# Kernel tuning notes

Hardware: AMD Instinct MI355X
Metric: run time of the kernel (lower is better)

The kernel has to match this reference:

```python
import jax, jax.numpy as jnp
import numpy as np

N_LEVELS = 16
N_FEATS = 2
LOG2_T = 19
TABLE_SIZE = 2 ** LOG2_T
BASE_RES = 16
PER_LEVEL_SCALE = 1.3819
N_PTS = 524288
# per-level grid resolutions (static)
RESOLUTIONS = np.floor(BASE_RES * PER_LEVEL_SCALE ** np.arange(N_LEVELS)).astype(np.float32)
# NGP spatial hash primes for 2D
PRIME0 = np.uint32(1)
PRIME1 = np.uint32(2654435761)
# corner offsets for bilinear interp: (0,0),(0,1),(1,0),(1,1)
CORNER_OFFS = np.array([[0, 0], [0, 1], [1, 0], [1, 1]], dtype=np.uint32)


def setup_inputs() -> dict:
    key = jax.random.key(0)
    k1, k2 = jax.random.split(key)
    pts = jax.random.uniform(k1, (N_PTS, 3), dtype=jnp.float32)  # coords in [0,1]
    # 3 planes x L levels x T entries x F features, small init like NGP (1e-4)
    tables = jax.random.normal(k2, (3, N_LEVELS, TABLE_SIZE, N_FEATS), dtype=jnp.float32) * 1e-4
    return {"pts": pts, "tables": tables}


def _encode_plane(coords, table):
    # coords: [N,2] in [0,1]; table: [L,T,F]
    L, T, F = table.shape
    res = jnp.asarray(RESOLUTIONS)  # [L]
    scaled = coords[None, :, :] * res[:, None, None]  # [L,N,2]
    x0 = jnp.floor(scaled)
    frac = scaled - x0  # [L,N,2]
    x0u = x0.astype(jnp.uint32)
    offs = jnp.asarray(CORNER_OFFS)  # [4,2]
    corners = x0u[:, :, None, :] + offs[None, None, :, :]  # [L,N,4,2]
    # NGP spatial hash with uint32 wraparound, then mod table size
    h = (corners[..., 0] * PRIME0) ^ (corners[..., 1] * PRIME1)  # [L,N,4] uint32
    idx = (h % jnp.uint32(T)).astype(jnp.int32)  # [L,N,4]
    feats = table[jnp.arange(L)[:, None, None], idx]  # [L,N,4,F]
    # bilinear weights: product over dims of frac (offset=1) or 1-frac (offset=0)
    fo = offs.astype(coords.dtype)  # [4,2]
    w = jnp.prod(jnp.where(fo[None, None] > 0, frac[:, :, None, :], 1.0 - frac[:, :, None, :]), axis=-1)  # [L,N,4]
    out = jnp.einsum('lnc,lncf->lnf', w, feats)  # [L,N,F]
    return out.transpose(1, 0, 2).reshape(coords.shape[0], L * F)  # [N, L*F]


def reference(pts, tables):
    # coordinate-pair planes: combinations of (0,1,2) taken 2 at a time
    coo_combs = [(0, 1), (0, 2), (1, 2)]
    interp_space = 1.0
    for ci, comb in enumerate(coo_combs):
        interp_space = interp_space * _encode_plane(pts[:, list(comb)], tables[ci])
    return interp_space  # [N, 32]
```

## Files before the change

### kernel.cpp

```cpp
#include <hip/hip_runtime.h>
#include <stdint.h>


#define NPTS   524288u
#define TSIZE  524288u
#define TMASK  0x7FFFFu
#define PRIME1 2654435761u

__constant__ float c_res[16] = {
    16.f, 22.f, 30.f, 42.f, 58.f, 80.f, 111.f, 153.f,
    212.f, 294.f, 406.f, 561.f, 775.f, 1072.f, 1481.f, 2047.f
};
__constant__ int c_resi[6] = {16, 22, 30, 42, 58, 80};

__constant__ uint16_t c_mid_lo[6]  = {0, 56, 0, 39, 78, 117};
__constant__ uint16_t c_mid_hiX[6] = {56, 112, 39, 78, 117, 154};

__global__ __launch_bounds__(512) void kplane_lds(
    const float* __restrict__ pts,
    const float2* __restrict__ tab,
    float2* __restrict__ ws)
{
    __shared__ float2 sm[6561];
    const uint32_t b     = blockIdx.x;
    const uint32_t gidx  = b >> 6;
    const uint32_t chunk = b & 63u;
    const uint32_t plane = gidx / 6u;
    const uint32_t lvl   = gidx - plane * 6u;
    const uint32_t g     = plane * 16u + lvl;
    const uint32_t R     = (uint32_t)c_resi[lvl] + 1u;
    const uint32_t E     = R * R;
    const float    res   = c_res[lvl];
    const uint32_t base  = g * TSIZE;
    const uint32_t t     = threadIdx.x;

    for (uint32_t i = t; i < E; i += 512u) {
        const uint32_t cx = i / R;
        const uint32_t cy = i - cx * R;
        sm[i] = tab[base + ((cx ^ (cy * PRIME1)) & TMASK)];
    }
    __syncthreads();

    const uint32_t c0  = (plane == 2u) ? 1u : 0u;
    const uint32_t c1  = (plane == 0u) ? 1u : 2u;
    const uint32_t pt0 = chunk * 8192u + t;

#pragma unroll 4
    for (uint32_t k = 0; k < 16u; ++k) {
        const uint32_t pt = pt0 + k * 512u;
        const float s0 = pts[pt * 3u + c0] * res;
        const float s1 = pts[pt * 3u + c1] * res;
        const float f0 = floorf(s0);
        const float f1 = floorf(s1);
        const float r0 = s0 - f0;
        const float r1 = s1 - f1;
        const uint32_t ci = (uint32_t)f0 * R + (uint32_t)f1;
        const float2 q00 = sm[ci];
        const float2 q01 = sm[ci + 1u];
        const float2 q10 = sm[ci + R];
        const float2 q11 = sm[ci + R + 1u];
        const float w00 = (1.f - r0) * (1.f - r1);
        const float w01 = (1.f - r0) * r1;
        const float w10 = r0 * (1.f - r1);
        const float w11 = r0 * r1;
        ws[g * NPTS + pt] = make_float2(
            w00 * q00.x + w01 * q01.x + w10 * q10.x + w11 * q11.x,
            w00 * q00.y + w01 * q01.y + w10 * q10.y + w11 * q11.y);
    }
}

__global__ __launch_bounds__(512) void kplane_mid(
    const float* __restrict__ pts,
    const float2* __restrict__ tab,
    float2* __restrict__ ws)
{
    __shared__ float2 sm[6400];
    const uint32_t b     = blockIdx.x;
    const uint32_t sg    = b >> 5;
    const uint32_t chunk = b & 31u;
    const uint32_t plane = sg / 6u;
    const uint32_t local = sg - plane * 6u;
    const uint32_t lvl   = (local < 2u) ? 6u : 7u;
    const uint32_t g     = plane * 16u + lvl;
    const uint32_t R     = (lvl == 6u) ? 112u : 154u;
    const uint32_t lo    = c_mid_lo[local];
    const uint32_t hiX   = c_mid_hiX[local];
    const uint32_t nrows = ((hiX < R ? hiX : R - 1u) - lo) + 1u;
    const uint32_t E     = nrows * R;
    const float    res   = c_res[lvl];
    const uint32_t base  = g * TSIZE;
    const uint32_t t     = threadIdx.x;

    for (uint32_t i = t; i < E; i += 512u) {
        const uint32_t rr = i / R;
        const uint32_t cy = i - rr * R;
        const uint32_t cx = lo + rr;
        sm[i] = tab[base + ((cx ^ (cy * PRIME1)) & TMASK)];
    }
    __syncthreads();

    const uint32_t c0  = (plane == 2u) ? 1u : 0u;
    const uint32_t c1  = (plane == 0u) ? 1u : 2u;
    const uint32_t pt0 = chunk * 16384u + t;

#pragma unroll 4
    for (uint32_t k = 0; k < 32u; ++k) {
        const uint32_t pt = pt0 + k * 512u;
        const float s0 = pts[pt * 3u + c0] * res;
        const float s1 = pts[pt * 3u + c1] * res;
        const float f0 = floorf(s0);
        const float f1 = floorf(s1);
        const uint32_t u0 = (uint32_t)f0;
        if (u0 >= lo && u0 < hiX) {
            const float r0 = s0 - f0;
            const float r1 = s1 - f1;
            const uint32_t ci = (u0 - lo) * R + (uint32_t)f1;
            const float2 q00 = sm[ci];
            const float2 q01 = sm[ci + 1u];
            const float2 q10 = sm[ci + R];
            const float2 q11 = sm[ci + R + 1u];
            const float w00 = (1.f - r0) * (1.f - r1);
            const float w01 = (1.f - r0) * r1;
            const float w10 = r0 * (1.f - r1);
            const float w11 = r0 * r1;
            ws[g * NPTS + pt] = make_float2(
                w00 * q00.x + w01 * q01.x + w10 * q10.x + w11 * q11.x,
                w00 * q00.y + w01 * q01.y + w10 * q10.y + w11 * q11.y);
        }
    }
}

__global__ __launch_bounds__(256) void kplane_hi(
    const float* __restrict__ pts,
    const float2* __restrict__ tab,
    float2* __restrict__ ws)
{
    const uint32_t b     = blockIdx.x;
    const uint32_t xcd   = b & 7u;
    const uint32_t s     = b >> 3;
    const uint32_t phase = s >> 9;
    const uint32_t chunk = s & 511u;
    const uint32_t plane = phase;
    const uint32_t lvl   = 8u + ((xcd + 3u * phase) & 7u);
    const uint32_t g     = plane * 16u + lvl;
    const float    res   = c_res[lvl];
    const uint32_t c0    = (plane == 2u) ? 1u : 0u;
    const uint32_t c1    = (plane == 0u) ? 1u : 2u;
    const uint32_t base  = g * TSIZE;
    const float4* __restrict__ tab4 = (const float4*)tab;
    const uint32_t b4    = g * (TSIZE / 2u);
    const uint32_t pt0   = chunk * 1024u + threadIdx.x;

    float4 P0[4], P1[4];
    float2 Q0[4], Q1[4];
    float  r0[4], r1[4];
    uint32_t sel0[4], sel1[4], oddm[4];

#pragma unroll
    for (int k = 0; k < 4; ++k) {
        const uint32_t pt = pt0 + (uint32_t)k * 256u;
        const float s0 = pts[pt * 3u + c0] * res;
        const float s1 = pts[pt * 3u + c1] * res;
        const float f0 = floorf(s0);
        const float f1 = floorf(s1);
        r0[k] = s0 - f0;
        r1[k] = s1 - f1;
        const uint32_t u0  = (uint32_t)f0;
        const uint32_t hy0 = (uint32_t)f1 * PRIME1;
        const uint32_t hy1 = hy0 + PRIME1;
        const uint32_t i00 = ( u0        ^ hy0) & TMASK;
        const uint32_t i01 = ( u0        ^ hy1) & TMASK;
        const uint32_t i10 = ((u0 + 1u)  ^ hy0) & TMASK;
        const uint32_t i11 = ((u0 + 1u)  ^ hy1) & TMASK;
        sel0[k] = i00 & 1u;
        sel1[k] = i01 & 1u;
        oddm[k] = u0 & 1u;
        P0[k] = tab4[b4 + (i00 >> 1)];
        P1[k] = tab4[b4 + (i01 >> 1)];
        Q0[k] = make_float2(0.f, 0.f);
        Q1[k] = make_float2(0.f, 0.f);
        if (oddm[k]) {
            Q0[k] = tab[base + i10];
            Q1[k] = tab[base + i11];
        }
    }
#pragma unroll
    for (int k = 0; k < 4; ++k) {
        const uint32_t pt = pt0 + (uint32_t)k * 256u;
        const float2 lo0 = make_float2(P0[k].x, P0[k].y);
        const float2 hi0 = make_float2(P0[k].z, P0[k].w);
        const float2 lo1 = make_float2(P1[k].x, P1[k].y);
        const float2 hi1 = make_float2(P1[k].z, P1[k].w);
        const float2 t00 = sel0[k] ? hi0 : lo0;
        const float2 t01 = sel1[k] ? hi1 : lo1;
        const float2 t10 = oddm[k] ? Q0[k] : (sel0[k] ? lo0 : hi0);
        const float2 t11 = oddm[k] ? Q1[k] : (sel1[k] ? lo1 : hi1);
        const float w00 = (1.f - r0[k]) * (1.f - r1[k]);
        const float w01 = (1.f - r0[k]) * r1[k];
        const float w10 = r0[k] * (1.f - r1[k]);
        const float w11 = r0[k] * r1[k];
        ws[g * NPTS + pt] = make_float2(
            w00 * t00.x + w01 * t01.x + w10 * t10.x + w11 * t11.x,
            w00 * t00.y + w01 * t01.y + w10 * t10.y + w11 * t11.y);
    }
}

__global__ __launch_bounds__(256) void kplane_combine(
    const float2* __restrict__ ws,
    float2* __restrict__ out)
{
    __shared__ float2 tile[16][65];
    const uint32_t pt0 = blockIdx.x * 64u;
    const uint32_t t   = threadIdx.x;
    const uint32_t lr  = t >> 6;
    const uint32_t ptl = t & 63u;

#pragma unroll
    for (int k = 0; k < 4; ++k) {
        const uint32_t lvl = (uint32_t)k * 4u + lr;
        const float2 a = ws[( 0u + lvl) * NPTS + pt0 + ptl];
        const float2 b = ws[(16u + lvl) * NPTS + pt0 + ptl];
        const float2 c = ws[(32u + lvl) * NPTS + pt0 + ptl];
        tile[lvl][ptl] = make_float2(a.x * b.x * c.x, a.y * b.y * c.y);
    }
    __syncthreads();
#pragma unroll
    for (int k = 0; k < 4; ++k) {
        const uint32_t e      = t + (uint32_t)k * 256u;
        const uint32_t out_lv = e & 15u;
        const uint32_t out_pt = e >> 4;
        out[(pt0 + out_pt) * 16u + out_lv] = tile[out_lv][out_pt];
    }
}

template <int P, bool FIRST>
__global__ __launch_bounds__(256) void kplane_pass(
    const float* __restrict__ pts,
    const float2* __restrict__ tab,
    float2* __restrict__ ws)
{
    const uint32_t b     = blockIdx.x;
    const uint32_t xcd   = b & 7u;
    const uint32_t s     = b >> 3;
    const uint32_t gi    = s >> 11;
    const uint32_t chunk = s & 2047u;
    const uint32_t lvl   = gi * 8u + xcd;
    const uint32_t pt    = chunk * 256u + threadIdx.x;

    constexpr int c0 = (P == 2) ? 1 : 0;
    constexpr int c1 = (P == 0) ? 1 : 2;

    const float a0  = pts[pt * 3u + c0];
    const float a1  = pts[pt * 3u + c1];
    const float res = c_res[lvl];

    const float s0 = a0 * res;
    const float s1 = a1 * res;
    const float f0 = floorf(s0);
    const float f1 = floorf(s1);
    const float r0 = s0 - f0;
    const float r1 = s1 - f1;
    const uint32_t u0 = (uint32_t)f0;
    const uint32_t hy0  = (uint32_t)f1 * PRIME1;
    const uint32_t hy1  = hy0 + PRIME1;
    const uint32_t base = ((uint32_t)P * 16u + lvl) * TSIZE;

    const float2 t00 = tab[base + (( u0       ^ hy0) & TMASK)];
    const float2 t01 = tab[base + (( u0       ^ hy1) & TMASK)];
    const float2 t10 = tab[base + (((u0 + 1u) ^ hy0) & TMASK)];
    const float2 t11 = tab[base + (((u0 + 1u) ^ hy1) & TMASK)];

    const float w00 = (1.f - r0) * (1.f - r1);
    const float w01 = (1.f - r0) * r1;
    const float w10 = r0 * (1.f - r1);
    const float w11 = r0 * r1;

    const float e0 = w00 * t00.x + w01 * t01.x + w10 * t10.x + w11 * t11.x;
    const float e1 = w00 * t00.y + w01 * t01.y + w10 * t10.y + w11 * t11.y;

    const uint32_t widx = lvl * NPTS + pt;
    if (FIRST) {
        ws[widx] = make_float2(e0, e1);
    } else {
        const float2 prev = ws[widx];
        ws[widx] = make_float2(prev.x * e0, prev.y * e1);
    }
}

__global__ __launch_bounds__(256) void kplane_transpose(
    const float2* __restrict__ ws, float2* __restrict__ out)
{
    const uint32_t tid = blockIdx.x * 256u + threadIdx.x;
    const uint32_t lvl = tid & 15u;
    const uint32_t pt  = tid >> 4;
    out[tid] = ws[lvl * NPTS + pt];
}

extern "C" void kernel_launch(void* const* d_in, const int* in_sizes, int n_in,
                              void* d_out, int out_size, void* d_ws, size_t ws_size,
                              hipStream_t stream) {
    const float*  pts = (const float*)d_in[0];
    const float2* tab = (const float2*)d_in[1];
    float2*       out = (float2*)d_out;

    const size_t wsA = (size_t)48 * NPTS * sizeof(float2);
    const size_t wsB = (size_t)16 * NPTS * sizeof(float2);
    dim3 block256(256u), block512(512u);

    if (ws_size >= wsA) {
        float2* ws = (float2*)d_ws;
        dim3 hgrid(3u * 8u * 512u);
        hipLaunchKernelGGL(kplane_hi, hgrid, block256, 0, stream, pts, tab, ws);
        dim3 mgrid(18u * 32u);
        hipLaunchKernelGGL(kplane_mid, mgrid, block512, 0, stream, pts, tab, ws);
        dim3 lgrid(18u * 64u);
        hipLaunchKernelGGL(kplane_lds, lgrid, block512, 0, stream, pts, tab, ws);
        dim3 cgrid(NPTS / 64u);
        hipLaunchKernelGGL(kplane_combine, cgrid, block256, 0, stream, ws, out);
    } else if (ws_size >= wsB) {
        float2* ws = (float2*)d_ws;
        dim3 grid(16u * (NPTS / 256u));
        hipLaunchKernelGGL((kplane_pass<0, true >), grid, block256, 0, stream, pts, tab, ws);
        hipLaunchKernelGGL((kplane_pass<1, false>), grid, block256, 0, stream, pts, tab, ws);
        hipLaunchKernelGGL((kplane_pass<2, false>), grid, block256, 0, stream, pts, tab, ws);
        dim3 tgrid((NPTS * 16u) / 256u);
        hipLaunchKernelGGL(kplane_transpose, tgrid, block256, 0, stream, ws, out);
    }
}
```

Before: 277.2 us.

## Pack plane coordinates and merge mid/low-level LDS kernels into one launch

Adds a pre-pass that repacks the xyz points into three per-plane float2 arrays, stored temporarily in the output buffer, so the gather kernels load coordinates with one contiguous 8-byte read. The separate mid-level and low-level LDS kernels are merged into a single launch. Levels 0-4 of each plane share one block that stages all five small grids in LDS and reuses each loaded point across them, while level 5 and levels 6-7 keep their own blocks with more points per block. A fallback monolithic kernel is added for small workspaces. The aim is fewer launches, less redundant point traffic and less LDS fill work, at the cost of an extra pack pass and fewer, longer-running blocks that may underfill the GPU.

```diff
diff --git a/kernel.cpp b/kernel.cpp
--- a/kernel.cpp
+++ b/kernel.cpp
@@ -11,127 +11,28 @@
     16.f, 22.f, 30.f, 42.f, 58.f, 80.f, 111.f, 153.f,
     212.f, 294.f, 406.f, 561.f, 775.f, 1072.f, 1481.f, 2047.f
 };
-__constant__ int c_resi[6] = {16, 22, 30, 42, 58, 80};
+
+__constant__ int c_RA[5]   = {17, 23, 31, 43, 59};
+__constant__ int c_offA[5] = {0, 289, 818, 1779, 3628};
 
 __constant__ uint16_t c_mid_lo[6]  = {0, 56, 0, 39, 78, 117};
 __constant__ uint16_t c_mid_hiX[6] = {56, 112, 39, 78, 117, 154};
 
-__global__ __launch_bounds__(512) void kplane_lds(
+__global__ __launch_bounds__(256) void kplane_pack(
     const float* __restrict__ pts,
-    const float2* __restrict__ tab,
-    float2* __restrict__ ws)
-{
-    __shared__ float2 sm[6561];
-    const uint32_t b     = blockIdx.x;
-    const uint32_t gidx  = b >> 6;
-    const uint32_t chunk = b & 63u;
-    const uint32_t plane = gidx / 6u;
-    const uint32_t lvl   = gidx - plane * 6u;
-    const uint32_t g     = plane * 16u + lvl;
-    const uint32_t R     = (uint32_t)c_resi[lvl] + 1u;
-    const uint32_t E     = R * R;
-    const float    res   = c_res[lvl];
-    const uint32_t base  = g * TSIZE;
-    const uint32_t t     = threadIdx.x;
-
-    for (uint32_t i = t; i < E; i += 512u) {
-        const uint32_t cx = i / R;
-        const uint32_t cy = i - cx * R;
-        sm[i] = tab[base + ((cx ^ (cy * PRIME1)) & TMASK)];
-    }
-    __syncthreads();
-
-    const uint32_t c0  = (plane == 2u) ? 1u : 0u;
-    const uint32_t c1  = (plane == 0u) ? 1u : 2u;
-    const uint32_t pt0 = chunk * 8192u + t;
-
-#pragma unroll 4
-    for (uint32_t k = 0; k < 16u; ++k) {
-        const uint32_t pt = pt0 + k * 512u;
-        const float s0 = pts[pt * 3u + c0] * res;
-        const float s1 = pts[pt * 3u + c1] * res;
-        const float f0 = floorf(s0);
-        const float f1 = floorf(s1);
-        const float r0 = s0 - f0;
-        const float r1 = s1 - f1;
-        const uint32_t ci = (uint32_t)f0 * R + (uint32_t)f1;
-        const float2 q00 = sm[ci];
-        const float2 q01 = sm[ci + 1u];
-        const float2 q10 = sm[ci + R];
-        const float2 q11 = sm[ci + R + 1u];
-        const float w00 = (1.f - r0) * (1.f - r1);
-        const float w01 = (1.f - r0) * r1;
-        const float w10 = r0 * (1.f - r1);
-        const float w11 = r0 * r1;
-        ws[g * NPTS + pt] = make_float2(
-            w00 * q00.x + w01 * q01.x + w10 * q10.x + w11 * q11.x,
-            w00 * q00.y + w01 * q01.y + w10 * q10.y + w11 * q11.y);
-    }
-}
-
-__global__ __launch_bounds__(512) void kplane_mid(
-    const float* __restrict__ pts,
-    const float2* __restrict__ tab,
-    float2* __restrict__ ws)
-{
-    __shared__ float2 sm[6400];
-    const uint32_t b     = blockIdx.x;
-    const uint32_t sg    = b >> 5;
-    const uint32_t chunk = b & 31u;
-    const uint32_t plane = sg / 6u;
-    const uint32_t local = sg - plane * 6u;
-    const uint32_t lvl   = (local < 2u) ? 6u : 7u;
-    const uint32_t g     = plane * 16u + lvl;
-    const uint32_t R     = (lvl == 6u) ? 112u : 154u;
-    const uint32_t lo    = c_mid_lo[local];
-    const uint32_t hiX   = c_mid_hiX[local];
-    const uint32_t nrows = ((hiX < R ? hiX : R - 1u) - lo) + 1u;
-    const uint32_t E     = nrows * R;
-    const float    res   = c_res[lvl];
-    const uint32_t base  = g * TSIZE;
-    const uint32_t t     = threadIdx.x;
-
-    for (uint32_t i = t; i < E; i += 512u) {
-        const uint32_t rr = i / R;
-        const uint32_t cy = i - rr * R;
-        const uint32_t cx = lo + rr;
-        sm[i] = tab[base + ((cx ^ (cy * PRIME1)) & TMASK)];
-    }
-    __syncthreads();
-
-    const uint32_t c0  = (plane == 2u) ? 1u : 0u;
-    const uint32_t c1  = (plane == 0u) ? 1u : 2u;
-    const uint32_t pt0 = chunk * 16384u + t;
-
-#pragma unroll 4
-    for (uint32_t k = 0; k < 32u; ++k) {
-        const uint32_t pt = pt0 + k * 512u;
-        const float s0 = pts[pt * 3u + c0] * res;
-        const float s1 = pts[pt * 3u + c1] * res;
-        const float f0 = floorf(s0);
-        const float f1 = floorf(s1);
-        const uint32_t u0 = (uint32_t)f0;
-        if (u0 >= lo && u0 < hiX) {
-            const float r0 = s0 - f0;
-            const float r1 = s1 - f1;
-            const uint32_t ci = (u0 - lo) * R + (uint32_t)f1;
-            const float2 q00 = sm[ci];
-            const float2 q01 = sm[ci + 1u];
-            const float2 q10 = sm[ci + R];
-            const float2 q11 = sm[ci + R + 1u];
-            const float w00 = (1.f - r0) * (1.f - r1);
-            const float w01 = (1.f - r0) * r1;
-            const float w10 = r0 * (1.f - r1);
-            const float w11 = r0 * r1;
-            ws[g * NPTS + pt] = make_float2(
-                w00 * q00.x + w01 * q01.x + w10 * q10.x + w11 * q11.x,
-                w00 * q00.y + w01 * q01.y + w10 * q10.y + w11 * q11.y);
-        }
-    }
+    float2* __restrict__ pts2)
+{
+    const uint32_t pt = blockIdx.x * 256u + threadIdx.x;
+    const float x = pts[pt * 3u + 0u];
+    const float y = pts[pt * 3u + 1u];
+    const float z = pts[pt * 3u + 2u];
+    pts2[            pt] = make_float2(x, y);
+    pts2[NPTS      + pt] = make_float2(x, z);
+    pts2[2u * NPTS + pt] = make_float2(y, z);
 }
 
 __global__ __launch_bounds__(256) void kplane_hi(
-    const float* __restrict__ pts,
+    const float2* __restrict__ pts2,
     const float2* __restrict__ tab,
     float2* __restrict__ ws)
 {
@@ -144,12 +45,11 @@
     const uint32_t lvl   = 8u + ((xcd + 3u * phase) & 7u);
     const uint32_t g     = plane * 16u + lvl;
     const float    res   = c_res[lvl];
-    const uint32_t c0    = (plane == 2u) ? 1u : 0u;
-    const uint32_t c1    = (plane == 0u) ? 1u : 2u;
     const uint32_t base  = g * TSIZE;
     const float4* __restrict__ tab4 = (const float4*)tab;
     const uint32_t b4    = g * (TSIZE / 2u);
     const uint32_t pt0   = chunk * 1024u + threadIdx.x;
+    const float2* __restrict__ pp = pts2 + (size_t)plane * NPTS;
 
     float4 P0[4], P1[4];
     float2 Q0[4], Q1[4];
@@ -159,8 +59,9 @@
 #pragma unroll
     for (int k = 0; k < 4; ++k) {
         const uint32_t pt = pt0 + (uint32_t)k * 256u;
-        const float s0 = pts[pt * 3u + c0] * res;
-        const float s1 = pts[pt * 3u + c1] * res;
+        const float2 c2 = pp[pt];
+        const float s0 = c2.x * res;
+        const float s1 = c2.y * res;
         const float f0 = floorf(s0);
         const float f1 = floorf(s1);
         r0[k] = s0 - f0;
@@ -205,6 +106,164 @@
     }
 }
 
+__global__ __launch_bounds__(512) void kplane_midlds(
+    const float2* __restrict__ pts2,
+    const float2* __restrict__ tab,
+    float2* __restrict__ ws)
+{
+    __shared__ float2 sm[7109];
+    const uint32_t b = blockIdx.x;
+    const uint32_t t = threadIdx.x;
+
+    if (b < 288u) {
+        const uint32_t sg    = b >> 4;
+        const uint32_t chunk = b & 15u;
+        const uint32_t plane = sg / 6u;
+        const uint32_t local = sg - plane * 6u;
+        const uint32_t lvl   = (local < 2u) ? 6u : 7u;
+        const uint32_t g     = plane * 16u + lvl;
+        const uint32_t R     = (lvl == 6u) ? 112u : 154u;
+        const uint32_t lo    = c_mid_lo[local];
+        const uint32_t hiX   = c_mid_hiX[local];
+        const uint32_t nrows = ((hiX < R ? hiX : R - 1u) - lo) + 1u;
+        const uint32_t E     = nrows * R;
+        const float    res   = c_res[lvl];
+        const uint32_t base  = g * TSIZE;
+
+        for (uint32_t i = t; i < E; i += 512u) {
+            const uint32_t rr = i / R;
+            const uint32_t cy = i - rr * R;
+            const uint32_t cx = lo + rr;
+            sm[i] = tab[base + ((cx ^ (cy * PRIME1)) & TMASK)];
+        }
+        __syncthreads();
+
+        const float2* __restrict__ pp = pts2 + (size_t)plane * NPTS;
+        const uint32_t pt0 = chunk * 32768u + t;
+
+#pragma unroll 4
+        for (uint32_t k = 0; k < 64u; ++k) {
+            const uint32_t pt = pt0 + k * 512u;
+            const float2 c2 = pp[pt];
+            const float s0 = c2.x * res;
+            const float s1 = c2.y * res;
+            const float f0 = floorf(s0);
+            const float f1 = floorf(s1);
+            const uint32_t u0 = (uint32_t)f0;
+            if (u0 >= lo && u0 < hiX) {
+                const float r0 = s0 - f0;
+                const float r1 = s1 - f1;
+                const uint32_t ci = (u0 - lo) * R + (uint32_t)f1;
+                const float2 q00 = sm[ci];
+                const float2 q01 = sm[ci + 1u];
+                const float2 q10 = sm[ci + R];
+                const float2 q11 = sm[ci + R + 1u];
+                const float w00 = (1.f - r0) * (1.f - r1);
+                const float w01 = (1.f - r0) * r1;
+                const float w10 = r0 * (1.f - r1);
+                const float w11 = r0 * r1;
+                ws[g * NPTS + pt] = make_float2(
+                    w00 * q00.x + w01 * q01.x + w10 * q10.x + w11 * q11.x,
+                    w00 * q00.y + w01 * q01.y + w10 * q10.y + w11 * q11.y);
+            }
+        }
+    } else if (b < 336u) {
+        const uint32_t idx   = b - 288u;
+        const uint32_t plane = idx >> 4;
+        const uint32_t chunk = idx & 15u;
+
+#pragma unroll
+        for (int l = 0; l < 5; ++l) {
+            const uint32_t R    = (uint32_t)c_RA[l];
+            const uint32_t E    = R * R;
+            const uint32_t off  = (uint32_t)c_offA[l];
+            const uint32_t base = (plane * 16u + (uint32_t)l) * TSIZE;
+            for (uint32_t i = t; i < E; i += 512u) {
+                const uint32_t cx = i / R;
+                const uint32_t cy = i - cx * R;
+                sm[off + i] = tab[base + ((cx ^ (cy * PRIME1)) & TMASK)];
+            }
+        }
+        __syncthreads();
+
+        const float2* __restrict__ pp = pts2 + (size_t)plane * NPTS;
+        const uint32_t pt0 = chunk * 32768u + t;
+
+#pragma unroll 2
+        for (uint32_t k = 0; k < 64u; ++k) {
+            const uint32_t pt = pt0 + k * 512u;
+            const float2 c2 = pp[pt];
+#pragma unroll
+            for (int l = 0; l < 5; ++l) {
+                const uint32_t R   = (uint32_t)c_RA[l];
+                const uint32_t off = (uint32_t)c_offA[l];
+                const float res = c_res[l];
+                const float s0 = c2.x * res;
+                const float s1 = c2.y * res;
+                const float f0 = floorf(s0);
+                const float f1 = floorf(s1);
+                const float r0 = s0 - f0;
+                const float r1 = s1 - f1;
+                const uint32_t ci = off + (uint32_t)f0 * R + (uint32_t)f1;
+                const float2 q00 = sm[ci];
+                const float2 q01 = sm[ci + 1u];
+                const float2 q10 = sm[ci + R];
+                const float2 q11 = sm[ci + R + 1u];
+                const float w00 = (1.f - r0) * (1.f - r1);
+                const float w01 = (1.f - r0) * r1;
+                const float w10 = r0 * (1.f - r1);
+                const float w11 = r0 * r1;
+                ws[(plane * 16u + (uint32_t)l) * NPTS + pt] = make_float2(
+                    w00 * q00.x + w01 * q01.x + w10 * q10.x + w11 * q11.x,
+                    w00 * q00.y + w01 * q01.y + w10 * q10.y + w11 * q11.y);
+            }
+        }
+    } else {
+        const uint32_t idx   = b - 336u;
+        const uint32_t plane = idx >> 4;
+        const uint32_t chunk = idx & 15u;
+        const uint32_t R     = 81u;
+        const uint32_t E     = 6561u;
+        const float    res   = 80.f;
+        const uint32_t g     = plane * 16u + 5u;
+        const uint32_t base  = g * TSIZE;
+
+        for (uint32_t i = t; i < E; i += 512u) {
+            const uint32_t cx = i / R;
+            const uint32_t cy = i - cx * R;
+            sm[i] = tab[base + ((cx ^ (cy * PRIME1)) & TMASK)];
+        }
+        __syncthreads();
+
+        const float2* __restrict__ pp = pts2 + (size_t)plane * NPTS;
+        const uint32_t pt0 = chunk * 32768u + t;
+
+#pragma unroll 4
+        for (uint32_t k = 0; k < 64u; ++k) {
+            const uint32_t pt = pt0 + k * 512u;
+            const float2 c2 = pp[pt];
+            const float s0 = c2.x * res;
+            const float s1 = c2.y * res;
+            const float f0 = floorf(s0);
+            const float f1 = floorf(s1);
+            const float r0 = s0 - f0;
+            const float r1 = s1 - f1;
+            const uint32_t ci = (uint32_t)f0 * R + (uint32_t)f1;
+            const float2 q00 = sm[ci];
+            const float2 q01 = sm[ci + 1u];
+            const float2 q10 = sm[ci + R];
+            const float2 q11 = sm[ci + R + 1u];
+            const float w00 = (1.f - r0) * (1.f - r1);
+            const float w01 = (1.f - r0) * r1;
+            const float w10 = r0 * (1.f - r1);
+            const float w11 = r0 * r1;
+            ws[g * NPTS + pt] = make_float2(
+                w00 * q00.x + w01 * q01.x + w10 * q10.x + w11 * q11.x,
+                w00 * q00.y + w01 * q01.y + w10 * q10.y + w11 * q11.y);
+        }
+    }
+}
+
 __global__ __launch_bounds__(256) void kplane_combine(
     const float2* __restrict__ ws,
     float2* __restrict__ out)
@@ -296,6 +355,47 @@
     out[tid] = ws[lvl * NPTS + pt];
 }
 
+__global__ __launch_bounds__(256) void kplane_mono(
+    const float* __restrict__ pts,
+    const float2* __restrict__ tab,
+    float2* __restrict__ out)
+{
+    const uint32_t tid = blockIdx.x * 256u + threadIdx.x;
+    const uint32_t pt  = tid >> 4;
+    const uint32_t lvl = tid & 15u;
+    const float x = pts[pt * 3u + 0u];
+    const float y = pts[pt * 3u + 1u];
+    const float z = pts[pt * 3u + 2u];
+    const float res = c_res[lvl];
+    const float a0[3] = {x, x, y};
+    const float a1[3] = {y, z, z};
+    float p0 = 1.f, p1 = 1.f;
+#pragma unroll
+    for (int pl = 0; pl < 3; ++pl) {
+        const float s0 = a0[pl] * res;
+        const float s1 = a1[pl] * res;
+        const float f0 = floorf(s0);
+        const float f1 = floorf(s1);
+        const float r0 = s0 - f0;
+        const float r1 = s1 - f1;
+        const uint32_t u0 = (uint32_t)f0;
+        const uint32_t hy0 = (uint32_t)f1 * PRIME1;
+        const uint32_t hy1 = hy0 + PRIME1;
+        const uint32_t base = ((uint32_t)pl * 16u + lvl) * TSIZE;
+        const float2 t00 = tab[base + (( u0       ^ hy0) & TMASK)];
+        const float2 t01 = tab[base + (( u0       ^ hy1) & TMASK)];
+        const float2 t10 = tab[base + (((u0 + 1u) ^ hy0) & TMASK)];
+        const float2 t11 = tab[base + (((u0 + 1u) ^ hy1) & TMASK)];
+        const float w00 = (1.f - r0) * (1.f - r1);
+        const float w01 = (1.f - r0) * r1;
+        const float w10 = r0 * (1.f - r1);
+        const float w11 = r0 * r1;
+        p0 *= w00 * t00.x + w01 * t01.x + w10 * t10.x + w11 * t11.x;
+        p1 *= w00 * t00.y + w01 * t01.y + w10 * t10.y + w11 * t11.y;
+    }
+    out[pt * 16u + lvl] = make_float2(p0, p1);
+}
+
 extern "C" void kernel_launch(void* const* d_in, const int* in_sizes, int n_in,
                               void* d_out, int out_size, void* d_ws, size_t ws_size,
                               hipStream_t stream) {
@@ -308,13 +408,14 @@
     dim3 block256(256u), block512(512u);
 
     if (ws_size >= wsA) {
-        float2* ws = (float2*)d_ws;
+        float2* ws   = (float2*)d_ws;
+        float2* pts2 = (float2*)d_out;
+        hipLaunchKernelGGL(kplane_pack, dim3(NPTS / 256u), block256, 0, stream,
+                           pts, pts2);
         dim3 hgrid(3u * 8u * 512u);
-        hipLaunchKernelGGL(kplane_hi, hgrid, block256, 0, stream, pts, tab, ws);
-        dim3 mgrid(18u * 32u);
-        hipLaunchKernelGGL(kplane_mid, mgrid, block512, 0, stream, pts, tab, ws);
-        dim3 lgrid(18u * 64u);
-        hipLaunchKernelGGL(kplane_lds, lgrid, block512, 0, stream, pts, tab, ws);
+        hipLaunchKernelGGL(kplane_hi, hgrid, block256, 0, stream, pts2, tab, ws);
+        dim3 mgrid(384u);
+        hipLaunchKernelGGL(kplane_midlds, mgrid, block512, 0, stream, pts2, tab, ws);
         dim3 cgrid(NPTS / 64u);
         hipLaunchKernelGGL(kplane_combine, cgrid, block256, 0, stream, ws, out);
     } else if (ws_size >= wsB) {
@@ -325,5 +426,8 @@
         hipLaunchKernelGGL((kplane_pass<2, false>), grid, block256, 0, stream, pts, tab, ws);
         dim3 tgrid((NPTS * 16u) / 256u);
         hipLaunchKernelGGL(kplane_transpose, tgrid, block256, 0, stream, ws, out);
-    }
-}
+    } else {
+        dim3 grid((NPTS * 16u) / 256u);
+        hipLaunchKernelGGL(kplane_mono, grid, block256, 0, stream, pts, tab, out);
+    }
+}
```

Result: slower. 288.9 us (+4.2%).
